# Performance work log

Measured on AMD Instinct MI355X. Metric: run time of the kernel, lower is better.

Reference implementation:

```python
import jax, jax.numpy as jnp
import numpy as np

EMB = 128
VAR_NF = 14
GRID_SIZE = 5
SPLINE_ORDER = 3
N_BASES = GRID_SIZE + SPLINE_ORDER  # 8
B, NV, NC = 32, 1024, 1024
EPS = 1e-5


def make_grid():
    # efficient-kan: grid = arange(-k, G+k+1)*h + grid_range[0], h = 2/G, range [-1, 1]
    h = 2.0 / GRID_SIZE
    return jnp.arange(-SPLINE_ORDER, GRID_SIZE + SPLINE_ORDER + 1, dtype=jnp.float32) * h - 1.0


def b_splines(x, g):
    # x: (N, in); g: (G + 2k + 1,) shared across features. Cox-de-Boor recursion.
    xe = x[..., None]
    bases = ((xe >= g[:-1]) & (xe < g[1:])).astype(x.dtype)  # (N, in, G+2k)
    for k in range(1, SPLINE_ORDER + 1):
        bases = ((xe - g[:-(k + 1)]) / (g[k:-1] - g[:-(k + 1)])) * bases[..., :-1] \
              + ((g[k + 1:] - xe) / (g[k + 1:] - g[1:-k])) * bases[..., 1:]
    return bases  # (N, in, G+k)


def kan_linear(x, base_w, spline_w, scaler, act):
    # base_w: (out, in); spline_w: (out, in, G+k); scaler: (out, in)
    g = make_grid()
    n_in = base_w.shape[1]
    xf = x.reshape(-1, n_in)
    base = act(xf) @ base_w.T
    bs = b_splines(xf, g)  # (N, in, 8)
    spline = jnp.einsum('nik,oik->no', bs, spline_w * scaler[..., None])
    return (base + spline).reshape(x.shape[:-1] + (base_w.shape[0],))


def layernorm(x, gamma, beta):
    mu = jnp.mean(x, axis=-1, keepdims=True)
    var = jnp.mean(jnp.square(x - mu), axis=-1, keepdims=True)
    return (x - mu) * jax.lax.rsqrt(var + EPS) * gamma + beta


def setup_inputs() -> dict:
    key = jax.random.key(0)
    ks = jax.random.split(key, 32)
    s = 0.05
    d = {}
    d['obs'] = jax.random.normal(ks[0], (B, NV, VAR_NF + NC), dtype=jnp.float32)
    d['W_emb'] = jax.random.normal(ks[1], (EMB, VAR_NF), dtype=jnp.float32) * s
    for i, kk in zip(range(1, 5), ks[2:6]):
        d[f'ln{i}_g'] = jnp.ones((EMB,), jnp.float32)
        d[f'ln{i}_b'] = jnp.zeros((EMB,), jnp.float32)
    for i, kk in zip(range(1, 4), ks[6:9]):
        d[f'lin{i}_w'] = jax.random.normal(kk, (EMB, EMB), dtype=jnp.float32) * s
        d[f'lin{i}_b'] = jnp.zeros((EMB,), jnp.float32)
    outs = [EMB, EMB, 1]
    for i in range(1, 4):
        o = outs[i - 1]
        k1, k2, k3 = jax.random.split(ks[9 + i], 3)
        d[f'kan{i}_base'] = jax.random.normal(k1, (o, EMB), dtype=jnp.float32) * s
        d[f'kan{i}_spline'] = jax.random.normal(k2, (o, EMB, N_BASES), dtype=jnp.float32) * s
        d[f'kan{i}_scaler'] = jnp.ones((o, EMB), jnp.float32)
    return d


def reference(obs, W_emb,
              ln1_g, ln1_b, ln2_g, ln2_b, ln3_g, ln3_b, ln4_g, ln4_b,
              lin1_w, lin1_b, lin2_w, lin2_b, lin3_w, lin3_b,
              kan1_base, kan1_spline, kan1_scaler,
              kan2_base, kan2_spline, kan2_scaler,
              kan3_base, kan3_spline, kan3_scaler):
    b, nv, col = obs.shape
    obs_all = obs.reshape(-1, col)
    obs1 = obs_all[:, :VAR_NF]                          # (b*nv, 14)
    a = obs_all[:, VAR_NF:].reshape(b, nv, col - VAR_NF)  # (b, nv, nc)
    x = (obs1 @ W_emb.T).reshape(b, nv, EMB)            # var embedding

    x_c = jnp.einsum('bvc,bve->bce', a, x)              # A^T x -> (b, nc, e)
    xc_c = jnp.tanh(layernorm(x_c, ln1_g, ln1_b))
    x_c = xc_c @ lin1_w.T + lin1_b
    x_c = jnp.einsum('bvc,bce->bve', a, x_c)            # A x_c -> (b, nv, e)
    x_c = jnp.tanh(layernorm(x_c, ln2_g, ln2_b))
    x_c_v = x_c + x
    x_c = x_c_v @ lin2_w.T + lin2_b
    x_c = jnp.einsum('bvc,bve->bce', a, x_c)            # A^T
    x_c = jnp.tanh(layernorm(x_c, ln3_g, ln3_b)) + xc_c
    x_c = x_c @ lin3_w.T + lin3_b
    x_c = jnp.einsum('bvc,bce->bve', a, x_c)            # A
    x = jnp.tanh(layernorm(x_c, ln4_g, ln4_b)) + x_c_v

    m = kan_linear(x, kan1_base, kan1_spline, kan1_scaler, jax.nn.silu)
    m = kan_linear(m, kan2_base, kan2_spline, kan2_scaler, jax.nn.silu)
    m = kan_linear(m, kan3_base, kan3_spline, kan3_scaler, jax.nn.sigmoid)
    return m * 0.6 + 0.2
```

## Files before the change

### kernel.cpp

```cpp
#include <hip/hip_runtime.h>
#include <math.h>

typedef __attribute__((ext_vector_type(8))) _Float16 h8;
typedef __attribute__((ext_vector_type(4))) _Float16 h4v;
typedef __attribute__((ext_vector_type(4))) float f4;

static constexpr int B_   = 32;
static constexpr int NV_  = 1024;
static constexpr int NC_  = 1024;
static constexpr int COL_ = 1038;
static constexpr int NF_  = 14;
static constexpr int E_   = 128;
static constexpr int ROWS_ = B_ * NV_;

__device__ __forceinline__ _Float16 f2h(float f) { return (_Float16)f; }

__device__ __forceinline__ void bsp(float x, float& P0, float& P1, float& P2,
                                    float& P3, int& c) {
  float u = fmaf(x, 2.5f, 5.5f);
  float cf = floorf(u);
  c = (int)cf;
  float t = u - cf;
  float t2 = t * t, t3 = t2 * t;
  float omt = 1.f - t;
  P0 = t3 * (1.f / 6.f);
  P1 = fmaf(-3.f, t3, fmaf(3.f, t2, fmaf(3.f, t, 1.f))) * (1.f / 6.f);
  P2 = fmaf(3.f, t3, fmaf(-6.f, t2, 4.f)) * (1.f / 6.f);
  P3 = omt * omt * omt * (1.f / 6.f);
}
__device__ __forceinline__ float bsel(int p, float P0, float P1, float P2, float P3) {
  float v = 0.f;
  v = (p == 0) ? P0 : v; v = (p == 1) ? P1 : v;
  v = (p == 2) ? P2 : v; v = (p == 3) ? P3 : v;
  return v;
}

__global__ void k_f32f16(const float* __restrict__ src, _Float16* __restrict__ dst, int n) {
  int idx = blockIdx.x * 256 + threadIdx.x;
  if (idx < n) dst[idx] = f2h(src[idx]);
}

__global__ void k_pack16(const float* __restrict__ base, const float* __restrict__ spline,
                         const float* __restrict__ scaler, _Float16* __restrict__ W9t) {
  int idx = blockIdx.x * 256 + threadIdx.x;
  int o = idx >> 11, k = idx & 2047, ch = k >> 4, q = k & 15;
  float v = 0.f;
  if (q == 0) v = base[o * 128 + ch];
  else if (q <= 8) v = spline[(o * 128 + ch) * 8 + q - 1] * scaler[o * 128 + ch];
  W9t[idx] = f2h(v);
}

__global__ void k_pack9k3(const float* __restrict__ base, const float* __restrict__ spline,
                          const float* __restrict__ scaler, float* __restrict__ w3) {
  int idx = blockIdx.x * 256 + threadIdx.x;
  if (idx >= 1152) return;
  int i = idx / 9, q = idx % 9;
  w3[idx] = (q == 0) ? base[i] : spline[i * 8 + q - 1] * scaler[i];
}

__global__ __launch_bounds__(256) void k_embed(const float* __restrict__ obs,
                                               const float* __restrict__ W_emb,
                                               float* __restrict__ X) {
  int t = threadIdx.x;
  int e = t & 127;
  size_t row = (size_t)blockIdx.x * 2 + (t >> 7);
  float w[NF_];
#pragma unroll
  for (int f = 0; f < NF_; ++f) w[f] = W_emb[e * NF_ + f];
  const float* orow = obs + row * COL_;
  float acc = 0.f;
#pragma unroll
  for (int f = 0; f < NF_; ++f) acc = fmaf(orow[f], w[f], acc);
  X[row * E_ + e] = acc;
}

__global__ __launch_bounds__(256) void k_transX(const float* __restrict__ Xf,
                                                _Float16* __restrict__ Xt) {
  int vt = blockIdx.x, et = blockIdx.y, b = blockIdx.z;
  __shared__ float tile[64][65];
  int t = threadIdx.x;
  int el = t & 63, q = t >> 6;
  const float* src = Xf + (size_t)b * 131072;
#pragma unroll 4
  for (int r = 0; r < 16; ++r) {
    int vl = q * 16 + r;
    tile[vl][el] = src[(size_t)(vt * 64 + vl) * 128 + et * 64 + el];
  }
  __syncthreads();
  _Float16* dst = Xt + (size_t)b * 131072;
#pragma unroll 4
  for (int r = 0; r < 16; ++r) {
    int el2 = q * 16 + r;
    dst[(size_t)(et * 64 + el2) * 1024 + vt * 64 + el] = f2h(tile[el][el2]);
  }
}

__global__ __launch_bounds__(256) void k_einsum_at(const float* __restrict__ obs,
                                                   const _Float16* __restrict__ Bt,
                                                   float* __restrict__ out) {
  int blk = blockIdx.x;
  int b = blk >> 3, ct = blk & 7;
  const float* obsb = obs + (size_t)b * NV_ * COL_;
  const _Float16* Btb = Bt + (size_t)b * 131072;
  float* outb = out + (size_t)b * 131072;
  int t = threadIdx.x, w = t >> 6, l = t & 63;
  int l15 = l & 15, g = l >> 4;
  int wR = (w >> 1) * 64, wC = (w & 1) * 64;
  int c0 = ct * 128;
  f4 acc[4][4] = {};

#pragma unroll 2
  for (int kk = 0; kk < NV_; kk += 32) {
    h8 af[4], bf[4];
#pragma unroll
    for (int m = 0; m < 4; ++m) {
      int c = c0 + wR + m * 16 + l15;
      const float* ap = obsb + (size_t)(kk + g * 8) * COL_ + NF_ + c;
#pragma unroll
      for (int j = 0; j < 8; ++j) af[m][j] = f2h(ap[(size_t)j * COL_]);
    }
#pragma unroll
    for (int n = 0; n < 4; ++n) {
      int e = wC + n * 16 + l15;
      bf[n] = *(const h8*)(Btb + (size_t)e * 1024 + kk + g * 8);
    }
#pragma unroll
    for (int m = 0; m < 4; ++m)
#pragma unroll
      for (int n = 0; n < 4; ++n)
        acc[m][n] = __builtin_amdgcn_mfma_f32_16x16x32_f16(af[m], bf[n], acc[m][n], 0, 0, 0);
  }
#pragma unroll
  for (int m = 0; m < 4; ++m)
#pragma unroll
    for (int n = 0; n < 4; ++n)
#pragma unroll
      for (int rr = 0; rr < 4; ++rr)
        outb[(size_t)(c0 + wR + m * 16 + g * 4 + rr) * 128 + wC + n * 16 + l15] = acc[m][n][rr];
}

__global__ __launch_bounds__(256) void k_einsum_a(const float* __restrict__ obs,
                                                  const _Float16* __restrict__ Bt,
                                                  float* __restrict__ out) {
  int blk = blockIdx.x;
  int b = blk >> 3, vt = blk & 7;
  const float* obsb = obs + (size_t)b * NV_ * COL_;
  const _Float16* Btb = Bt + (size_t)b * 131072;
  float* outb = out + (size_t)b * 131072;
  int t = threadIdx.x, w = t >> 6, l = t & 63;
  int l15 = l & 15, g = l >> 4;
  int wR = (w >> 1) * 64, wC = (w & 1) * 64;
  int v0 = vt * 128;
  f4 acc[4][4] = {};

#pragma unroll 2
  for (int kk = 0; kk < NC_; kk += 32) {
    h8 af[4], bf[4];
#pragma unroll
    for (int m = 0; m < 4; ++m) {
      int v = v0 + wR + m * 16 + l15;
      const float2* ap = (const float2*)(obsb + (size_t)v * COL_ + NF_ + kk + g * 8);
      float2 p0 = ap[0], p1 = ap[1], p2 = ap[2], p3 = ap[3];
      af[m][0] = f2h(p0.x); af[m][1] = f2h(p0.y);
      af[m][2] = f2h(p1.x); af[m][3] = f2h(p1.y);
      af[m][4] = f2h(p2.x); af[m][5] = f2h(p2.y);
      af[m][6] = f2h(p3.x); af[m][7] = f2h(p3.y);
    }
#pragma unroll
    for (int n = 0; n < 4; ++n) {
      int e = wC + n * 16 + l15;
      bf[n] = *(const h8*)(Btb + (size_t)e * 1024 + kk + g * 8);
    }
#pragma unroll
    for (int m = 0; m < 4; ++m)
#pragma unroll
      for (int n = 0; n < 4; ++n)
        acc[m][n] = __builtin_amdgcn_mfma_f32_16x16x32_f16(af[m], bf[n], acc[m][n], 0, 0, 0);
  }
#pragma unroll
  for (int m = 0; m < 4; ++m)
#pragma unroll
    for (int n = 0; n < 4; ++n)
#pragma unroll
      for (int rr = 0; rr < 4; ++rr)
        outb[(size_t)(v0 + wR + m * 16 + g * 4 + rr) * 128 + wC + n * 16 + l15] = acc[m][n][rr];
}

__global__ __launch_bounds__(256) void k_lin(const _Float16* __restrict__ Inb,
                                             const _Float16* __restrict__ Wb,
                                             const float* __restrict__ bias,
                                             _Float16* __restrict__ outT) {
  int row0 = blockIdx.x * 128;
  int b = row0 >> 10, vb = row0 & 1023;
  int t = threadIdx.x, w = t >> 6, l = t & 63;
  int l15 = l & 15, g = l >> 4;
  int wR = (w >> 1) * 64, wC = (w & 1) * 64;
  f4 acc[4][4] = {};

#pragma unroll
  for (int kk = 0; kk < 128; kk += 32) {
    h8 af[4], bf[4];
#pragma unroll
    for (int m = 0; m < 4; ++m)
      af[m] = *(const h8*)(Inb + (size_t)(row0 + wR + m * 16 + l15) * 128 + kk + g * 8);
#pragma unroll
    for (int n = 0; n < 4; ++n)
      bf[n] = *(const h8*)(Wb + (size_t)(wC + n * 16 + l15) * 128 + kk + g * 8);
#pragma unroll
    for (int m = 0; m < 4; ++m)
#pragma unroll
      for (int n = 0; n < 4; ++n)
        acc[m][n] = __builtin_amdgcn_mfma_f32_16x16x32_f16(af[m], bf[n], acc[m][n], 0, 0, 0);
  }
#pragma unroll
  for (int m = 0; m < 4; ++m)
#pragma unroll
    for (int n = 0; n < 4; ++n) {
      int col = wC + n * 16 + l15;
      float bv = bias[col];
      h4v sv;
#pragma unroll
      for (int rr = 0; rr < 4; ++rr) sv[rr] = f2h(acc[m][n][rr] + bv);
      *(h4v*)(outT + (size_t)b * 131072 + (size_t)col * 1024 + vb + wR + m * 16 + g * 4) = sv;
    }
}

__global__ __launch_bounds__(256) void k_ln(const float* in, const float* gam,
                                            const float* bet, const float* addp,
                                            float* outf, _Float16* outb) {
  size_t wid = ((size_t)blockIdx.x * 256 + threadIdx.x) >> 6;
  int lane = threadIdx.x & 63;
  const float* r = in + wid * E_;
  float x0 = r[lane], x1 = r[lane + 64];
  float s = x0 + x1;
  float s2 = x0 * x0 + x1 * x1;
#pragma unroll
  for (int off = 32; off >= 1; off >>= 1) {
    s += __shfl_xor(s, off);
    s2 += __shfl_xor(s2, off);
  }
  float mu = s * (1.0f / 128.0f);
  float var = s2 * (1.0f / 128.0f) - mu * mu;
  float rstd = rsqrtf(var + 1e-5f);
  float t0 = tanhf((x0 - mu) * rstd * gam[lane] + bet[lane]);
  float t1 = tanhf((x1 - mu) * rstd * gam[lane + 64] + bet[lane + 64]);
  if (addp) {
    t0 += addp[wid * E_ + lane];
    t1 += addp[wid * E_ + lane + 64];
  }
  outf[wid * E_ + lane] = t0;
  outf[wid * E_ + lane + 64] = t1;
  outb[wid * E_ + lane] = f2h(t0);
  outb[wid * E_ + lane + 64] = f2h(t1);
}

template <int ACT>
__global__ __launch_bounds__(256) void k_kan(const float* __restrict__ Xin,
                                             const _Float16* __restrict__ W9t,
                                             float* __restrict__ out) {
  int row0 = blockIdx.x * 128;
  __shared__ float xs[128 * 129];
  __shared__ _Float16 As[128 * 64];
  int t = threadIdx.x, w = t >> 6, l = t & 63;
  int l15 = l & 15, g = l >> 4;
  int wR = (w >> 1) * 64, wC = (w & 1) * 64;
  int rr_ = t & 127, sub = t >> 7;

#pragma unroll
  for (int p = 0; p < 16; ++p) {
    int idx4 = (p * 256 + t) * 4;
    int r = idx4 >> 7, c4 = idx4 & 127;
    const f4 v = *(const f4*)(Xin + (size_t)(row0 + r) * 128 + c4);
    xs[r * 129 + c4] = v[0]; xs[r * 129 + c4 + 1] = v[1];
    xs[r * 129 + c4 + 2] = v[2]; xs[r * 129 + c4 + 3] = v[3];
  }
  __syncthreads();

  f4 acc[4][4] = {};
  for (int chunk = 0; chunk < 32; ++chunk) {
#pragma unroll
    for (int s = 0; s < 2; ++s) {
      int cl = sub * 2 + s;
      int ch = chunk * 4 + cl;
      float x = xs[rr_ * 129 + ch];
      float act;
      if (ACT == 0) act = x / (1.f + __expf(-x));
      else          act = 1.f / (1.f + __expf(-x));
      float P0, P1, P2, P3; int c;
      bsp(x, P0, P1, P2, P3, c);
      h8 lo, hi;
      lo[0] = f2h(act);
#pragma unroll
      for (int j = 0; j < 7; ++j) lo[1 + j] = f2h(bsel(c - j, P0, P1, P2, P3));
      hi[0] = f2h(bsel(c - 7, P0, P1, P2, P3));
#pragma unroll
      for (int q = 1; q < 8; ++q) hi[q] = (_Float16)0.f;
      int sw = (rr_ & 7) << 4;
      *(h8*)((char*)As + rr_ * 128 + ((cl * 32) ^ sw)) = lo;
      *(h8*)((char*)As + rr_ * 128 + ((cl * 32 + 16) ^ sw)) = hi;
    }
    __syncthreads();
#pragma unroll
    for (int ks = 0; ks < 2; ++ks) {
      h8 af[4], bf[4];
#pragma unroll
      for (int m = 0; m < 4; ++m) {
        int r = wR + m * 16 + l15;
        int cb = (ks * 64 + g * 16) ^ ((r & 7) << 4);
        af[m] = *(h8*)((char*)As + r * 128 + cb);
      }
#pragma unroll
      for (int n = 0; n < 4; ++n) {
        int col = wC + n * 16 + l15;
        bf[n] = *(const h8*)(W9t + (size_t)col * 2048 + chunk * 64 + ks * 32 + g * 8);
      }
#pragma unroll
      for (int m = 0; m < 4; ++m)
#pragma unroll
        for (int n = 0; n < 4; ++n)
          acc[m][n] = __builtin_amdgcn_mfma_f32_16x16x32_f16(af[m], bf[n], acc[m][n], 0, 0, 0);
    }
    __syncthreads();
  }
#pragma unroll
  for (int m = 0; m < 4; ++m)
#pragma unroll
    for (int n = 0; n < 4; ++n)
#pragma unroll
      for (int rr = 0; rr < 4; ++rr)
        out[(size_t)(row0 + wR + m * 16 + g * 4 + rr) * 128 + wC + n * 16 + l15] = acc[m][n][rr];
}

__global__ __launch_bounds__(256) void k_kan3(const float* __restrict__ xin,
                                              const float* __restrict__ w3,
                                              float* __restrict__ out) {
  size_t wid = ((size_t)blockIdx.x * 256 + threadIdx.x) >> 6;
  int lane = threadIdx.x & 63;
  const float* xr = xin + wid * E_;
  float s = 0.f;
#pragma unroll
  for (int half = 0; half < 2; ++half) {
    int i = lane + half * 64;
    float x = xr[i];
    float sig = 1.f / (1.f + __expf(-x));
    const float* ww = w3 + i * 9;
    s = fmaf(sig, ww[0], s);
    float P0, P1, P2, P3; int c;
    bsp(x, P0, P1, P2, P3, c);
#pragma unroll
    for (int j = 0; j < 8; ++j) s = fmaf(bsel(c - j, P0, P1, P2, P3), ww[1 + j], s);
  }
#pragma unroll
  for (int off = 32; off >= 1; off >>= 1) s += __shfl_xor(s, off);
  if (lane == 0) out[wid] = s * 0.6f + 0.2f;
}

extern "C" void kernel_launch(void* const* d_in, const int* in_sizes, int n_in,
                              void* d_out, int out_size, void* d_ws, size_t ws_size,
                              hipStream_t stream) {
  (void)in_sizes; (void)n_in; (void)out_size; (void)ws_size;
  const float* obs   = (const float*)d_in[0];
  const float* W_emb = (const float*)d_in[1];
  const float* ln1_g = (const float*)d_in[2];
  const float* ln1_b = (const float*)d_in[3];
  const float* ln2_g = (const float*)d_in[4];
  const float* ln2_b = (const float*)d_in[5];
  const float* ln3_g = (const float*)d_in[6];
  const float* ln3_b = (const float*)d_in[7];
  const float* ln4_g = (const float*)d_in[8];
  const float* ln4_b = (const float*)d_in[9];
  const float* lin1_w = (const float*)d_in[10];
  const float* lin1_b = (const float*)d_in[11];
  const float* lin2_w = (const float*)d_in[12];
  const float* lin2_b = (const float*)d_in[13];
  const float* lin3_w = (const float*)d_in[14];
  const float* lin3_b = (const float*)d_in[15];
  const float* kan1_base = (const float*)d_in[16];
  const float* kan1_spline = (const float*)d_in[17];
  const float* kan1_scaler = (const float*)d_in[18];
  const float* kan2_base = (const float*)d_in[19];
  const float* kan2_spline = (const float*)d_in[20];
  const float* kan2_scaler = (const float*)d_in[21];
  const float* kan3_base = (const float*)d_in[22];
  const float* kan3_spline = (const float*)d_in[23];
  const float* kan3_scaler = (const float*)d_in[24];

  char* wsb = (char*)d_ws;
  const size_t MB16 = (size_t)1 << 24;
  const size_t MB8  = (size_t)1 << 23;
  float* Xf  = (float*)(wsb);
  float* XCC = (float*)(wsb + MB16);
  float* XCV = (float*)(wsb + 2 * MB16);
  float* T1  = (float*)(wsb + 3 * MB16);
  _Float16* LTt = (_Float16*)(wsb + 4 * MB16);
  _Float16* LNb = (_Float16*)(wsb + 4 * MB16 + MB8);
  char*  p   = wsb + 4 * MB16 + 2 * MB8;
  _Float16* W9t1 = (_Float16*)p;      p += 128 * 2048 * 2;
  _Float16* W9t2 = (_Float16*)p;      p += 128 * 2048 * 2;
  _Float16* Wb1  = (_Float16*)p;      p += 128 * 128 * 2;
  _Float16* Wb2  = (_Float16*)p;      p += 128 * 128 * 2;
  _Float16* Wb3  = (_Float16*)p;      p += 128 * 128 * 2;
  float* w3v  = (float*)p;

  k_f32f16<<<64, 256, 0, stream>>>(lin1_w, Wb1, 16384);
  k_f32f16<<<64, 256, 0, stream>>>(lin2_w, Wb2, 16384);
  k_f32f16<<<64, 256, 0, stream>>>(lin3_w, Wb3, 16384);
  k_pack16<<<1024, 256, 0, stream>>>(kan1_base, kan1_spline, kan1_scaler, W9t1);
  k_pack16<<<1024, 256, 0, stream>>>(kan2_base, kan2_spline, kan2_scaler, W9t2);
  k_pack9k3<<<5, 256, 0, stream>>>(kan3_base, kan3_spline, kan3_scaler, w3v);

  k_embed<<<ROWS_ / 2, 256, 0, stream>>>(obs, W_emb, Xf);
  k_transX<<<dim3(16, 2, 32), 256, 0, stream>>>(Xf, LTt);
  k_einsum_at<<<256, 256, 0, stream>>>(obs, LTt, T1);
  k_ln<<<ROWS_ / 4, 256, 0, stream>>>(T1, ln1_g, ln1_b, nullptr, XCC, LNb);
  k_lin<<<256, 256, 0, stream>>>(LNb, Wb1, lin1_b, LTt);
  k_einsum_a<<<256, 256, 0, stream>>>(obs, LTt, T1);
  k_ln<<<ROWS_ / 4, 256, 0, stream>>>(T1, ln2_g, ln2_b, Xf, XCV, LNb);
  k_lin<<<256, 256, 0, stream>>>(LNb, Wb2, lin2_b, LTt);
  k_einsum_at<<<256, 256, 0, stream>>>(obs, LTt, T1);
  k_ln<<<ROWS_ / 4, 256, 0, stream>>>(T1, ln3_g, ln3_b, XCC, XCC, LNb);
  k_lin<<<256, 256, 0, stream>>>(LNb, Wb3, lin3_b, LTt);
  k_einsum_a<<<256, 256, 0, stream>>>(obs, LTt, T1);
  k_ln<<<ROWS_ / 4, 256, 0, stream>>>(T1, ln4_g, ln4_b, XCV, XCC, LNb);
  k_kan<0><<<256, 256, 0, stream>>>(XCC, W9t1, T1);
  k_kan<0><<<256, 256, 0, stream>>>(T1, W9t2, XCV);
  k_kan3<<<ROWS_ / 4, 256, 0, stream>>>(XCV, w3v, (float*)d_out);
}
```

Before: 626.3 us.

## Precompute fp16 A and A^T once and feed einsums and KAN with fp16

Adds a prep kernel that converts the adjacency block of obs into fp16 in both row-major and transposed layouts, so all four einsums use a generic kernel with contiguous vector loads instead of rereading fp32 obs with strided scalar gathers. The KAN layers now consume and produce fp16 activations, halving their traffic. This needs an extra ~128MB of workspace (gated on ws_size, with a fallback to the old path) and a one-off conversion pass, and it lowers the precision of the KAN intermediates.

```diff
diff --git a/kernel.cpp b/kernel.cpp
--- a/kernel.cpp
+++ b/kernel.cpp
@@ -1,5 +1,6 @@
 #include <hip/hip_runtime.h>
 #include <math.h>
+#include <stdint.h>
 
 typedef __attribute__((ext_vector_type(8))) _Float16 h8;
 typedef __attribute__((ext_vector_type(4))) _Float16 h4v;
@@ -58,6 +59,32 @@
   w3[idx] = (q == 0) ? base[i] : spline[i * 8 + q - 1] * scaler[i];
 }
 
+__global__ __launch_bounds__(256) void k_prepA(const float* __restrict__ obs,
+                                               _Float16* __restrict__ A16,
+                                               _Float16* __restrict__ AT16) {
+  int ct = blockIdx.x, vt = blockIdx.y, b = blockIdx.z;
+  __shared__ _Float16 tile[64][65];
+  int t = threadIdx.x;
+  int cl = t & 63, rq = t >> 6;
+  const float* ob = obs + (size_t)b * NV_ * COL_ + NF_;
+  _Float16* a16b = A16 + (size_t)b * NV_ * 1024;
+#pragma unroll 4
+  for (int r = 0; r < 16; ++r) {
+    int vl = rq * 16 + r;
+    int v = vt * 64 + vl, c = ct * 64 + cl;
+    _Float16 h = f2h(ob[(size_t)v * COL_ + c]);
+    a16b[(size_t)v * 1024 + c] = h;
+    tile[vl][cl] = h;
+  }
+  __syncthreads();
+  _Float16* at16b = AT16 + (size_t)b * NC_ * 1024;
+#pragma unroll 4
+  for (int r = 0; r < 16; ++r) {
+    int crow = rq * 16 + r;
+    at16b[(size_t)(ct * 64 + crow) * 1024 + vt * 64 + cl] = tile[cl][crow];
+  }
+}
+
 __global__ __launch_bounds__(256) void k_embed(const float* __restrict__ obs,
                                                const float* __restrict__ W_emb,
                                                float* __restrict__ X) {
@@ -93,6 +120,44 @@
     int el2 = q * 16 + r;
     dst[(size_t)(et * 64 + el2) * 1024 + vt * 64 + el] = f2h(tile[el][el2]);
   }
+}
+
+__global__ __launch_bounds__(256) void k_einsum16(const _Float16* __restrict__ Ar,
+                                                  const _Float16* __restrict__ Bt,
+                                                  float* __restrict__ out) {
+  int blk = blockIdx.x;
+  int b = blk >> 3, rt = blk & 7;
+  const _Float16* Arb = Ar + (size_t)b * 1024 * 1024;
+  const _Float16* Btb = Bt + (size_t)b * 131072;
+  float* outb = out + (size_t)b * 131072;
+  int t = threadIdx.x, w = t >> 6, l = t & 63;
+  int l15 = l & 15, g = l >> 4;
+  int wR = (w >> 1) * 64, wC = (w & 1) * 64;
+  int r0 = rt * 128;
+  f4 acc[4][4] = {};
+
+#pragma unroll 2
+  for (int kk = 0; kk < 1024; kk += 32) {
+    h8 af[4], bf[4];
+#pragma unroll
+    for (int m = 0; m < 4; ++m)
+      af[m] = *(const h8*)(Arb + (size_t)(r0 + wR + m * 16 + l15) * 1024 + kk + g * 8);
+#pragma unroll
+    for (int n = 0; n < 4; ++n)
+      bf[n] = *(const h8*)(Btb + (size_t)(wC + n * 16 + l15) * 1024 + kk + g * 8);
+#pragma unroll
+    for (int m = 0; m < 4; ++m)
+#pragma unroll
+      for (int n = 0; n < 4; ++n)
+        acc[m][n] = __builtin_amdgcn_mfma_f32_16x16x32_f16(af[m], bf[n], acc[m][n], 0, 0, 0);
+  }
+#pragma unroll
+  for (int m = 0; m < 4; ++m)
+#pragma unroll
+    for (int n = 0; n < 4; ++n)
+#pragma unroll
+      for (int rr = 0; rr < 4; ++rr)
+        outb[(size_t)(r0 + wR + m * 16 + g * 4 + rr) * 128 + wC + n * 16 + l15] = acc[m][n][rr];
 }
 
 __global__ __launch_bounds__(256) void k_einsum_at(const float* __restrict__ obs,
@@ -108,7 +173,6 @@
   int wR = (w >> 1) * 64, wC = (w & 1) * 64;
   int c0 = ct * 128;
   f4 acc[4][4] = {};
-
 #pragma unroll 2
   for (int kk = 0; kk < NV_; kk += 32) {
     h8 af[4], bf[4];
@@ -120,10 +184,8 @@
       for (int j = 0; j < 8; ++j) af[m][j] = f2h(ap[(size_t)j * COL_]);
     }
 #pragma unroll
-    for (int n = 0; n < 4; ++n) {
-      int e = wC + n * 16 + l15;
-      bf[n] = *(const h8*)(Btb + (size_t)e * 1024 + kk + g * 8);
-    }
+    for (int n = 0; n < 4; ++n)
+      bf[n] = *(const h8*)(Btb + (size_t)(wC + n * 16 + l15) * 1024 + kk + g * 8);
 #pragma unroll
     for (int m = 0; m < 4; ++m)
 #pragma unroll
@@ -152,7 +214,6 @@
   int wR = (w >> 1) * 64, wC = (w & 1) * 64;
   int v0 = vt * 128;
   f4 acc[4][4] = {};
-
 #pragma unroll 2
   for (int kk = 0; kk < NC_; kk += 32) {
     h8 af[4], bf[4];
@@ -167,10 +228,8 @@
       af[m][6] = f2h(p3.x); af[m][7] = f2h(p3.y);
     }
 #pragma unroll
-    for (int n = 0; n < 4; ++n) {
-      int e = wC + n * 16 + l15;
-      bf[n] = *(const h8*)(Btb + (size_t)e * 1024 + kk + g * 8);
-    }
+    for (int n = 0; n < 4; ++n)
+      bf[n] = *(const h8*)(Btb + (size_t)(wC + n * 16 + l15) * 1024 + kk + g * 8);
 #pragma unroll
     for (int m = 0; m < 4; ++m)
 #pragma unroll
@@ -255,11 +314,11 @@
 }
 
 template <int ACT>
-__global__ __launch_bounds__(256) void k_kan(const float* __restrict__ Xin,
+__global__ __launch_bounds__(256) void k_kan(const _Float16* __restrict__ Xin,
                                              const _Float16* __restrict__ W9t,
-                                             float* __restrict__ out) {
+                                             _Float16* __restrict__ out) {
   int row0 = blockIdx.x * 128;
-  __shared__ float xs[128 * 129];
+  __shared__ _Float16 xs[128 * 136];
   __shared__ _Float16 As[128 * 64];
   int t = threadIdx.x, w = t >> 6, l = t & 63;
   int l15 = l & 15, g = l >> 4;
@@ -267,12 +326,10 @@
   int rr_ = t & 127, sub = t >> 7;
 
 #pragma unroll
-  for (int p = 0; p < 16; ++p) {
-    int idx4 = (p * 256 + t) * 4;
-    int r = idx4 >> 7, c4 = idx4 & 127;
-    const f4 v = *(const f4*)(Xin + (size_t)(row0 + r) * 128 + c4);
-    xs[r * 129 + c4] = v[0]; xs[r * 129 + c4 + 1] = v[1];
-    xs[r * 129 + c4 + 2] = v[2]; xs[r * 129 + c4 + 3] = v[3];
+  for (int p = 0; p < 8; ++p) {
+    int idx8 = (p * 256 + t) * 8;
+    int r = idx8 >> 7, c8 = idx8 & 127;
+    *(h8*)(&xs[r * 136 + c8]) = *(const h8*)(Xin + (size_t)(row0 + r) * 128 + c8);
   }
   __syncthreads();
 
@@ -282,7 +339,7 @@
     for (int s = 0; s < 2; ++s) {
       int cl = sub * 2 + s;
       int ch = chunk * 4 + cl;
-      float x = xs[rr_ * 129 + ch];
+      float x = (float)xs[rr_ * 136 + ch];
       float act;
       if (ACT == 0) act = x / (1.f + __expf(-x));
       else          act = 1.f / (1.f + __expf(-x));
@@ -328,20 +385,21 @@
     for (int n = 0; n < 4; ++n)
 #pragma unroll
       for (int rr = 0; rr < 4; ++rr)
-        out[(size_t)(row0 + wR + m * 16 + g * 4 + rr) * 128 + wC + n * 16 + l15] = acc[m][n][rr];
-}
-
-__global__ __launch_bounds__(256) void k_kan3(const float* __restrict__ xin,
+        out[(size_t)(row0 + wR + m * 16 + g * 4 + rr) * 128 + wC + n * 16 + l15] =
+            f2h(acc[m][n][rr]);
+}
+
+__global__ __launch_bounds__(256) void k_kan3(const _Float16* __restrict__ xin,
                                               const float* __restrict__ w3,
                                               float* __restrict__ out) {
   size_t wid = ((size_t)blockIdx.x * 256 + threadIdx.x) >> 6;
   int lane = threadIdx.x & 63;
-  const float* xr = xin + wid * E_;
+  const _Float16* xr = xin + wid * E_;
   float s = 0.f;
 #pragma unroll
   for (int half = 0; half < 2; ++half) {
     int i = lane + half * 64;
-    float x = xr[i];
+    float x = (float)xr[i];
     float sig = 1.f / (1.f + __expf(-x));
     const float* ww = w3 + i * 9;
     s = fmaf(sig, ww[0], s);
@@ -358,7 +416,7 @@
 extern "C" void kernel_launch(void* const* d_in, const int* in_sizes, int n_in,
                               void* d_out, int out_size, void* d_ws, size_t ws_size,
                               hipStream_t stream) {
-  (void)in_sizes; (void)n_in; (void)out_size; (void)ws_size;
+  (void)in_sizes; (void)n_in; (void)out_size;
   const float* obs   = (const float*)d_in[0];
   const float* W_emb = (const float*)d_in[1];
   const float* ln1_g = (const float*)d_in[2];
@@ -400,7 +458,12 @@
   _Float16* Wb1  = (_Float16*)p;      p += 128 * 128 * 2;
   _Float16* Wb2  = (_Float16*)p;      p += 128 * 128 * 2;
   _Float16* Wb3  = (_Float16*)p;      p += 128 * 128 * 2;
-  float* w3v  = (float*)p;
+  float* w3v  = (float*)p;            p += 1152 * 4;
+  p = (char*)(((uintptr_t)p + 255) & ~(uintptr_t)255);
+  _Float16* A16  = (_Float16*)p;
+  _Float16* AT16 = (_Float16*)(p + (size_t)NV_ * 1024 * 2 * B_);
+  size_t need = (size_t)(p - wsb) + 2 * (size_t)B_ * NV_ * 1024 * 2;
+  const bool fast = ws_size >= need;
 
   k_f32f16<<<64, 256, 0, stream>>>(lin1_w, Wb1, 16384);
   k_f32f16<<<64, 256, 0, stream>>>(lin2_w, Wb2, 16384);
@@ -408,21 +471,26 @@
   k_pack16<<<1024, 256, 0, stream>>>(kan1_base, kan1_spline, kan1_scaler, W9t1);
   k_pack16<<<1024, 256, 0, stream>>>(kan2_base, kan2_spline, kan2_scaler, W9t2);
   k_pack9k3<<<5, 256, 0, stream>>>(kan3_base, kan3_spline, kan3_scaler, w3v);
+  if (fast) k_prepA<<<dim3(16, 16, 32), 256, 0, stream>>>(obs, A16, AT16);
 
   k_embed<<<ROWS_ / 2, 256, 0, stream>>>(obs, W_emb, Xf);
   k_transX<<<dim3(16, 2, 32), 256, 0, stream>>>(Xf, LTt);
-  k_einsum_at<<<256, 256, 0, stream>>>(obs, LTt, T1);
+  if (fast) k_einsum16<<<256, 256, 0, stream>>>(AT16, LTt, T1);
+  else      k_einsum_at<<<256, 256, 0, stream>>>(obs, LTt, T1);
   k_ln<<<ROWS_ / 4, 256, 0, stream>>>(T1, ln1_g, ln1_b, nullptr, XCC, LNb);
   k_lin<<<256, 256, 0, stream>>>(LNb, Wb1, lin1_b, LTt);
-  k_einsum_a<<<256, 256, 0, stream>>>(obs, LTt, T1);
+  if (fast) k_einsum16<<<256, 256, 0, stream>>>(A16, LTt, T1);
+  else      k_einsum_a<<<256, 256, 0, stream>>>(obs, LTt, T1);
   k_ln<<<ROWS_ / 4, 256, 0, stream>>>(T1, ln2_g, ln2_b, Xf, XCV, LNb);
   k_lin<<<256, 256, 0, stream>>>(LNb, Wb2, lin2_b, LTt);
-  k_einsum_at<<<256, 256, 0, stream>>>(obs, LTt, T1);
+  if (fast) k_einsum16<<<256, 256, 0, stream>>>(AT16, LTt, T1);
+  else      k_einsum_at<<<256, 256, 0, stream>>>(obs, LTt, T1);
   k_ln<<<ROWS_ / 4, 256, 0, stream>>>(T1, ln3_g, ln3_b, XCC, XCC, LNb);
   k_lin<<<256, 256, 0, stream>>>(LNb, Wb3, lin3_b, LTt);
-  k_einsum_a<<<256, 256, 0, stream>>>(obs, LTt, T1);
+  if (fast) k_einsum16<<<256, 256, 0, stream>>>(A16, LTt, T1);
+  else      k_einsum_a<<<256, 256, 0, stream>>>(obs, LTt, T1);
   k_ln<<<ROWS_ / 4, 256, 0, stream>>>(T1, ln4_g, ln4_b, XCV, XCC, LNb);
-  k_kan<0><<<256, 256, 0, stream>>>(XCC, W9t1, T1);
-  k_kan<0><<<256, 256, 0, stream>>>(T1, W9t2, XCV);
-  k_kan3<<<ROWS_ / 4, 256, 0, stream>>>(XCV, w3v, (float*)d_out);
-}
+  k_kan<0><<<256, 256, 0, stream>>>(LNb, W9t1, LTt);
+  k_kan<0><<<256, 256, 0, stream>>>(LTt, W9t2, LNb);
+  k_kan3<<<ROWS_ / 4, 256, 0, stream>>>(LNb, w3v, (float*)d_out);
+}
```

After: 694.3 us. +10.9%, slower.

## Shrink einsum and KAN tiles for more blocks, pass KAN activations in fp16

Applied to the files above, without the earlier changes.

The four adjacency einsum kernels now use 64x64 output tiles with a 2x2 MFMA block per wave, launching 1024 blocks instead of 256. This is meant to improve occupancy and latency hiding on the many-CU GPU, at the cost of re-reading the strided fp32 obs A-operand more often. The KAN kernels use 64-row tiles (512 blocks) and read and write fp16 activations instead of fp32. Layernorm skips the fp32 output when it is unused, which cuts memory traffic but lowers the precision of the KAN inputs and intermediates.

```diff
diff --git a/kernel.cpp b/kernel.cpp
--- a/kernel.cpp
+++ b/kernel.cpp
@@ -1,5 +1,6 @@
 #include <hip/hip_runtime.h>
 #include <math.h>
+#include <stdint.h>
 
 typedef __attribute__((ext_vector_type(8))) _Float16 h8;
 typedef __attribute__((ext_vector_type(4))) _Float16 h4v;
@@ -99,66 +100,68 @@
                                                    const _Float16* __restrict__ Bt,
                                                    float* __restrict__ out) {
   int blk = blockIdx.x;
-  int b = blk >> 3, ct = blk & 7;
+  int b = blk >> 5, rest = blk & 31;
+  int mt = rest >> 1, nt = rest & 1;
   const float* obsb = obs + (size_t)b * NV_ * COL_;
   const _Float16* Btb = Bt + (size_t)b * 131072;
   float* outb = out + (size_t)b * 131072;
   int t = threadIdx.x, w = t >> 6, l = t & 63;
   int l15 = l & 15, g = l >> 4;
-  int wR = (w >> 1) * 64, wC = (w & 1) * 64;
-  int c0 = ct * 128;
-  f4 acc[4][4] = {};
+  int wm = w >> 1, wn = w & 1;
+  int c0 = mt * 64 + wm * 32;
+  int e0 = nt * 64 + wn * 32;
+  f4 acc[2][2] = {};
 
 #pragma unroll 2
   for (int kk = 0; kk < NV_; kk += 32) {
-    h8 af[4], bf[4];
-#pragma unroll
-    for (int m = 0; m < 4; ++m) {
-      int c = c0 + wR + m * 16 + l15;
+    h8 af[2], bf[2];
+#pragma unroll
+    for (int m = 0; m < 2; ++m) {
+      int c = c0 + m * 16 + l15;
       const float* ap = obsb + (size_t)(kk + g * 8) * COL_ + NF_ + c;
 #pragma unroll
       for (int j = 0; j < 8; ++j) af[m][j] = f2h(ap[(size_t)j * COL_]);
     }
 #pragma unroll
-    for (int n = 0; n < 4; ++n) {
-      int e = wC + n * 16 + l15;
-      bf[n] = *(const h8*)(Btb + (size_t)e * 1024 + kk + g * 8);
-    }
-#pragma unroll
-    for (int m = 0; m < 4; ++m)
-#pragma unroll
-      for (int n = 0; n < 4; ++n)
+    for (int n = 0; n < 2; ++n)
+      bf[n] = *(const h8*)(Btb + (size_t)(e0 + n * 16 + l15) * 1024 + kk + g * 8);
+#pragma unroll
+    for (int m = 0; m < 2; ++m)
+#pragma unroll
+      for (int n = 0; n < 2; ++n)
         acc[m][n] = __builtin_amdgcn_mfma_f32_16x16x32_f16(af[m], bf[n], acc[m][n], 0, 0, 0);
   }
 #pragma unroll
-  for (int m = 0; m < 4; ++m)
-#pragma unroll
-    for (int n = 0; n < 4; ++n)
+  for (int m = 0; m < 2; ++m)
+#pragma unroll
+    for (int n = 0; n < 2; ++n)
 #pragma unroll
       for (int rr = 0; rr < 4; ++rr)
-        outb[(size_t)(c0 + wR + m * 16 + g * 4 + rr) * 128 + wC + n * 16 + l15] = acc[m][n][rr];
+        outb[(size_t)(c0 + m * 16 + g * 4 + rr) * 128 + e0 + n * 16 + l15] = acc[m][n][rr];
 }
 
 __global__ __launch_bounds__(256) void k_einsum_a(const float* __restrict__ obs,
                                                   const _Float16* __restrict__ Bt,
                                                   float* __restrict__ out) {
   int blk = blockIdx.x;
-  int b = blk >> 3, vt = blk & 7;
+  int b = blk >> 5, rest = blk & 31;
+  int mt = rest >> 1, nt = rest & 1;
   const float* obsb = obs + (size_t)b * NV_ * COL_;
   const _Float16* Btb = Bt + (size_t)b * 131072;
   float* outb = out + (size_t)b * 131072;
   int t = threadIdx.x, w = t >> 6, l = t & 63;
   int l15 = l & 15, g = l >> 4;
-  int wR = (w >> 1) * 64, wC = (w & 1) * 64;
-  int v0 = vt * 128;
-  f4 acc[4][4] = {};
+  int wm = w >> 1, wn = w & 1;
+  int v0 = mt * 64 + wm * 32;
+  int e0 = nt * 64 + wn * 32;
+  f4 acc[2][2] = {};
 
 #pragma unroll 2
   for (int kk = 0; kk < NC_; kk += 32) {
-    h8 af[4], bf[4];
-#pragma unroll
-    for (int m = 0; m < 4; ++m) {
-      int v = v0 + wR + m * 16 + l15;
+    h8 af[2], bf[2];
+#pragma unroll
+    for (int m = 0; m < 2; ++m) {
+      int v = v0 + m * 16 + l15;
       const float2* ap = (const float2*)(obsb + (size_t)v * COL_ + NF_ + kk + g * 8);
       float2 p0 = ap[0], p1 = ap[1], p2 = ap[2], p3 = ap[3];
       af[m][0] = f2h(p0.x); af[m][1] = f2h(p0.y);
@@ -167,23 +170,21 @@
       af[m][6] = f2h(p3.x); af[m][7] = f2h(p3.y);
     }
 #pragma unroll
-    for (int n = 0; n < 4; ++n) {
-      int e = wC + n * 16 + l15;
-      bf[n] = *(const h8*)(Btb + (size_t)e * 1024 + kk + g * 8);
-    }
-#pragma unroll
-    for (int m = 0; m < 4; ++m)
-#pragma unroll
-      for (int n = 0; n < 4; ++n)
+    for (int n = 0; n < 2; ++n)
+      bf[n] = *(const h8*)(Btb + (size_t)(e0 + n * 16 + l15) * 1024 + kk + g * 8);
+#pragma unroll
+    for (int m = 0; m < 2; ++m)
+#pragma unroll
+      for (int n = 0; n < 2; ++n)
         acc[m][n] = __builtin_amdgcn_mfma_f32_16x16x32_f16(af[m], bf[n], acc[m][n], 0, 0, 0);
   }
 #pragma unroll
-  for (int m = 0; m < 4; ++m)
-#pragma unroll
-    for (int n = 0; n < 4; ++n)
+  for (int m = 0; m < 2; ++m)
+#pragma unroll
+    for (int n = 0; n < 2; ++n)
 #pragma unroll
       for (int rr = 0; rr < 4; ++rr)
-        outb[(size_t)(v0 + wR + m * 16 + g * 4 + rr) * 128 + wC + n * 16 + l15] = acc[m][n][rr];
+        outb[(size_t)(v0 + m * 16 + g * 4 + rr) * 128 + e0 + n * 16 + l15] = acc[m][n][rr];
 }
 
 __global__ __launch_bounds__(256) void k_lin(const _Float16* __restrict__ Inb,
@@ -248,41 +249,40 @@
     t0 += addp[wid * E_ + lane];
     t1 += addp[wid * E_ + lane + 64];
   }
-  outf[wid * E_ + lane] = t0;
-  outf[wid * E_ + lane + 64] = t1;
+  if (outf) {
+    outf[wid * E_ + lane] = t0;
+    outf[wid * E_ + lane + 64] = t1;
+  }
   outb[wid * E_ + lane] = f2h(t0);
   outb[wid * E_ + lane + 64] = f2h(t1);
 }
 
 template <int ACT>
-__global__ __launch_bounds__(256) void k_kan(const float* __restrict__ Xin,
+__global__ __launch_bounds__(256) void k_kan(const _Float16* __restrict__ Xin,
                                              const _Float16* __restrict__ W9t,
-                                             float* __restrict__ out) {
-  int row0 = blockIdx.x * 128;
-  __shared__ float xs[128 * 129];
-  __shared__ _Float16 As[128 * 64];
+                                             _Float16* __restrict__ out) {
+  int row0 = blockIdx.x * 64;
+  __shared__ _Float16 xs[64 * 136];
+  __shared__ _Float16 As[64 * 128];
   int t = threadIdx.x, w = t >> 6, l = t & 63;
   int l15 = l & 15, g = l >> 4;
-  int wR = (w >> 1) * 64, wC = (w & 1) * 64;
-  int rr_ = t & 127, sub = t >> 7;
-
-#pragma unroll
-  for (int p = 0; p < 16; ++p) {
-    int idx4 = (p * 256 + t) * 4;
-    int r = idx4 >> 7, c4 = idx4 & 127;
-    const f4 v = *(const f4*)(Xin + (size_t)(row0 + r) * 128 + c4);
-    xs[r * 129 + c4] = v[0]; xs[r * 129 + c4 + 1] = v[1];
-    xs[r * 129 + c4 + 2] = v[2]; xs[r * 129 + c4 + 3] = v[3];
+  int rr_ = t & 63, sub = t >> 6;
+
+#pragma unroll
+  for (int p = 0; p < 4; ++p) {
+    int idx8 = (p * 256 + t) * 8;
+    int r = idx8 >> 7, c8 = idx8 & 127;
+    *(h8*)(&xs[r * 136 + c8]) = *(const h8*)(Xin + (size_t)(row0 + r) * 128 + c8);
   }
   __syncthreads();
 
-  f4 acc[4][4] = {};
-  for (int chunk = 0; chunk < 32; ++chunk) {
+  f4 acc[4][2] = {};
+  for (int chunk = 0; chunk < 16; ++chunk) {
 #pragma unroll
     for (int s = 0; s < 2; ++s) {
       int cl = sub * 2 + s;
-      int ch = chunk * 4 + cl;
-      float x = xs[rr_ * 129 + ch];
+      int ch = chunk * 8 + cl;
+      float x = (float)xs[rr_ * 136 + ch];
       float act;
       if (ACT == 0) act = x / (1.f + __expf(-x));
       else          act = 1.f / (1.f + __expf(-x));
@@ -296,28 +296,28 @@
 #pragma unroll
       for (int q = 1; q < 8; ++q) hi[q] = (_Float16)0.f;
       int sw = (rr_ & 7) << 4;
-      *(h8*)((char*)As + rr_ * 128 + ((cl * 32) ^ sw)) = lo;
-      *(h8*)((char*)As + rr_ * 128 + ((cl * 32 + 16) ^ sw)) = hi;
+      *(h8*)((char*)As + rr_ * 256 + ((cl * 32) ^ sw)) = lo;
+      *(h8*)((char*)As + rr_ * 256 + ((cl * 32 + 16) ^ sw)) = hi;
     }
     __syncthreads();
 #pragma unroll
-    for (int ks = 0; ks < 2; ++ks) {
-      h8 af[4], bf[4];
+    for (int ks = 0; ks < 4; ++ks) {
+      h8 af[4], bf[2];
 #pragma unroll
       for (int m = 0; m < 4; ++m) {
-        int r = wR + m * 16 + l15;
+        int r = m * 16 + l15;
         int cb = (ks * 64 + g * 16) ^ ((r & 7) << 4);
-        af[m] = *(h8*)((char*)As + r * 128 + cb);
+        af[m] = *(h8*)((char*)As + r * 256 + cb);
       }
 #pragma unroll
-      for (int n = 0; n < 4; ++n) {
-        int col = wC + n * 16 + l15;
-        bf[n] = *(const h8*)(W9t + (size_t)col * 2048 + chunk * 64 + ks * 32 + g * 8);
+      for (int n = 0; n < 2; ++n) {
+        int col = w * 32 + n * 16 + l15;
+        bf[n] = *(const h8*)(W9t + (size_t)col * 2048 + chunk * 128 + ks * 32 + g * 8);
       }
 #pragma unroll
       for (int m = 0; m < 4; ++m)
 #pragma unroll
-        for (int n = 0; n < 4; ++n)
+        for (int n = 0; n < 2; ++n)
           acc[m][n] = __builtin_amdgcn_mfma_f32_16x16x32_f16(af[m], bf[n], acc[m][n], 0, 0, 0);
     }
     __syncthreads();
@@ -325,23 +325,24 @@
 #pragma unroll
   for (int m = 0; m < 4; ++m)
 #pragma unroll
-    for (int n = 0; n < 4; ++n)
+    for (int n = 0; n < 2; ++n)
 #pragma unroll
       for (int rr = 0; rr < 4; ++rr)
-        out[(size_t)(row0 + wR + m * 16 + g * 4 + rr) * 128 + wC + n * 16 + l15] = acc[m][n][rr];
-}
-
-__global__ __launch_bounds__(256) void k_kan3(const float* __restrict__ xin,
+        out[(size_t)(row0 + m * 16 + g * 4 + rr) * 128 + w * 32 + n * 16 + l15] =
+            f2h(acc[m][n][rr]);
+}
+
+__global__ __launch_bounds__(256) void k_kan3(const _Float16* __restrict__ xin,
                                               const float* __restrict__ w3,
                                               float* __restrict__ out) {
   size_t wid = ((size_t)blockIdx.x * 256 + threadIdx.x) >> 6;
   int lane = threadIdx.x & 63;
-  const float* xr = xin + wid * E_;
+  const _Float16* xr = xin + wid * E_;
   float s = 0.f;
 #pragma unroll
   for (int half = 0; half < 2; ++half) {
     int i = lane + half * 64;
-    float x = xr[i];
+    float x = (float)xr[i];
     float sig = 1.f / (1.f + __expf(-x));
     const float* ww = w3 + i * 9;
     s = fmaf(sig, ww[0], s);
@@ -411,18 +412,18 @@
 
   k_embed<<<ROWS_ / 2, 256, 0, stream>>>(obs, W_emb, Xf);
   k_transX<<<dim3(16, 2, 32), 256, 0, stream>>>(Xf, LTt);
-  k_einsum_at<<<256, 256, 0, stream>>>(obs, LTt, T1);
+  k_einsum_at<<<1024, 256, 0, stream>>>(obs, LTt, T1);
   k_ln<<<ROWS_ / 4, 256, 0, stream>>>(T1, ln1_g, ln1_b, nullptr, XCC, LNb);
   k_lin<<<256, 256, 0, stream>>>(LNb, Wb1, lin1_b, LTt);
-  k_einsum_a<<<256, 256, 0, stream>>>(obs, LTt, T1);
+  k_einsum_a<<<1024, 256, 0, stream>>>(obs, LTt, T1);
   k_ln<<<ROWS_ / 4, 256, 0, stream>>>(T1, ln2_g, ln2_b, Xf, XCV, LNb);
   k_lin<<<256, 256, 0, stream>>>(LNb, Wb2, lin2_b, LTt);
-  k_einsum_at<<<256, 256, 0, stream>>>(obs, LTt, T1);
-  k_ln<<<ROWS_ / 4, 256, 0, stream>>>(T1, ln3_g, ln3_b, XCC, XCC, LNb);
+  k_einsum_at<<<1024, 256, 0, stream>>>(obs, LTt, T1);
+  k_ln<<<ROWS_ / 4, 256, 0, stream>>>(T1, ln3_g, ln3_b, XCC, nullptr, LNb);
   k_lin<<<256, 256, 0, stream>>>(LNb, Wb3, lin3_b, LTt);
-  k_einsum_a<<<256, 256, 0, stream>>>(obs, LTt, T1);
-  k_ln<<<ROWS_ / 4, 256, 0, stream>>>(T1, ln4_g, ln4_b, XCV, XCC, LNb);
-  k_kan<0><<<256, 256, 0, stream>>>(XCC, W9t1, T1);
-  k_kan<0><<<256, 256, 0, stream>>>(T1, W9t2, XCV);
-  k_kan3<<<ROWS_ / 4, 256, 0, stream>>>(XCV, w3v, (float*)d_out);
-}
+  k_einsum_a<<<1024, 256, 0, stream>>>(obs, LTt, T1);
+  k_ln<<<ROWS_ / 4, 256, 0, stream>>>(T1, ln4_g, ln4_b, XCV, nullptr, LNb);
+  k_kan<0><<<512, 256, 0, stream>>>(LNb, W9t1, LTt);
+  k_kan<0><<<512, 256, 0, stream>>>(LTt, W9t2, LNb);
+  k_kan3<<<ROWS_ / 4, 256, 0, stream>>>(LNb, w3v, (float*)d_out);
+}
```

Measured after the change: 689.2 us. +10.0%, slower.
